# Performance work log

Hardware: AMD Instinct MI355X
Metric: run time of the kernel (lower is better)

## Reference

```python
import jax, jax.numpy as jnp
import numpy as np

N_HEADS, D_MODEL, D_HEAD = 16, 1024, 64
INIT_STD = 0.02


def setup_inputs() -> dict:
    key = jax.random.key(0)
    ks = jax.random.split(key, 5)
    x = jax.random.normal(ks[0], (4, 2048, D_MODEL), dtype=jnp.float32)
    W_Q = jax.random.normal(ks[1], (N_HEADS, D_MODEL, D_HEAD), dtype=jnp.float32) * INIT_STD
    W_K = jax.random.normal(ks[2], (N_HEADS, D_MODEL, D_HEAD), dtype=jnp.float32) * INIT_STD
    W_V = jax.random.normal(ks[3], (N_HEADS, D_MODEL, D_HEAD), dtype=jnp.float32) * INIT_STD
    W_O = jax.random.normal(ks[4], (N_HEADS, D_HEAD, D_MODEL), dtype=jnp.float32) * INIT_STD
    b_Q = jnp.zeros((N_HEADS, D_HEAD), dtype=jnp.float32)
    b_K = jnp.zeros((N_HEADS, D_HEAD), dtype=jnp.float32)
    b_V = jnp.zeros((N_HEADS, D_HEAD), dtype=jnp.float32)
    b_O = jnp.zeros((D_MODEL,), dtype=jnp.float32)
    return {"normalized_resid_pre": x, "W_Q": W_Q, "W_K": W_K, "W_V": W_V,
            "W_O": W_O, "b_Q": b_Q, "b_K": b_K, "b_V": b_V, "b_O": b_O}


def reference(normalized_resid_pre, W_Q, W_K, W_V, W_O, b_Q, b_K, b_V, b_O):
    x = normalized_resid_pre  # [b, s, d_model]
    q = jnp.einsum('bsm,hmd->bshd', x, W_Q) + b_Q  # [b, s, h, d_head]
    k = jnp.einsum('bsm,hmd->bshd', x, W_K) + b_K
    v = jnp.einsum('bsm,hmd->bshd', x, W_V) + b_V
    scores = jnp.einsum('bqhd,bkhd->bhqk', q, k) / jnp.sqrt(jnp.float32(D_HEAD))
    S = x.shape[1]
    causal = jnp.tril(jnp.ones((S, S), dtype=bool))  # keep key_pos <= query_pos
    scores = jnp.where(causal, scores, jnp.finfo(scores.dtype).min)
    pattern = jax.nn.softmax(scores, axis=-1)  # [b, h, q, k]
    z = jnp.einsum('bhqk,bkhd->bqhd', pattern, v)
    attn_out = jnp.einsum('bqhd,hdm->bqm', z, W_O) + b_O
    return attn_out
```

## Files before the change

### kernel.cpp

```cpp
#include <hip/hip_runtime.h>
#include <hip/hip_bf16.h>
#include <math.h>

typedef __bf16 bf16_t;
typedef bf16_t bf16x8 __attribute__((ext_vector_type(8)));
typedef float f32x4 __attribute__((ext_vector_type(4)));

#define BB 4
#define SS 2048
#define HH 16
#define DMODEL 1024
#define DHEAD 64

__device__ inline unsigned short f2bf(float f) {
    union { __hip_bfloat16 h; unsigned short u; } cvt;
    cvt.h = __float2bfloat16(f);
    return cvt.u;
}

__device__ __forceinline__ void gll16(const unsigned short* g, unsigned short* l) {
    __builtin_amdgcn_global_load_lds(
        (const __attribute__((address_space(1))) unsigned int*)(g),
        (__attribute__((address_space(3))) unsigned int*)(l), 16, 0, 0);
}


__global__ void pack_x(const float* __restrict__ x, unsigned short* __restrict__ xb) {
    int i = blockIdx.x * 256 + threadIdx.x;
    const float4 v = ((const float4*)x)[i];
    unsigned short o[4] = { f2bf(v.x), f2bf(v.y), f2bf(v.z), f2bf(v.w) };
    *(uint2*)(xb + 4 * (size_t)i) = *(uint2*)o;
}

__global__ void pack_wqkv(const float* __restrict__ wq, const float* __restrict__ wk,
                          const float* __restrict__ wv, unsigned short* __restrict__ out) {
    int idx = blockIdx.x * 256 + threadIdx.x;
    int k  = idx & 1023;
    int n  = idx >> 10;
    int mat = n >> 10;
    int n1 = n & 1023;
    int h = n1 >> 6, d = n1 & 63;
    const float* w = (mat == 0) ? wq : (mat == 1) ? wk : wv;
    out[idx] = f2bf(w[(h << 16) + (k << 6) + d]);
}

__global__ void pack_wo(const float* __restrict__ wo, unsigned short* __restrict__ out) {
    int idx = blockIdx.x * 256 + threadIdx.x;
    int k = idx & 1023, n = idx >> 10;
    out[idx] = f2bf(wo[(k << 10) + n]);
}


__global__ __launch_bounds__(256) void gemm_qkv(
    const unsigned short* __restrict__ xb,
    const unsigned short* __restrict__ wT,
    const float* __restrict__ bq, const float* __restrict__ bk, const float* __restrict__ bv,
    unsigned short* __restrict__ qws, unsigned short* __restrict__ kws,
    unsigned short* __restrict__ vtw)
{
    __shared__ __align__(16) unsigned short lA[128 * 32];
    __shared__ __align__(16) unsigned short lB[128 * 32];
    const int t = threadIdx.x;
    const int lane = t & 63;
    const int w = t >> 6;
    const int quad = lane >> 4;
    const int l15 = lane & 15;
    const int n0 = blockIdx.x * 128;
    const int m0 = blockIdx.y * 128;
    const int wm = (w >> 1) * 64;
    const int wn = (w & 1) * 64;
    const int mat = n0 >> 10;

    f32x4 acc[4][4] = {};

    const int srow = w * 16 + (lane >> 2);
    const int scol = (lane & 3) * 8;
    const unsigned short* Ag0 = xb + (size_t)(m0 + srow) * 1024 + scol;
    const unsigned short* Ag1 = Ag0 + (size_t)64 * 1024;
    const unsigned short* Bg0 = wT + (size_t)(n0 + srow) * 1024 + scol;
    const unsigned short* Bg1 = Bg0 + (size_t)64 * 1024;
    unsigned short* lA0 = lA + (w * 16) * 32;
    unsigned short* lA1 = lA + (64 + w * 16) * 32;
    unsigned short* lB0 = lB + (w * 16) * 32;
    unsigned short* lB1 = lB + (64 + w * 16) * 32;

    if (mat != 2) {
        for (int kt = 0; kt < 1024; kt += 32) {
            __syncthreads();
            gll16(Ag0 + kt, lA0);
            gll16(Ag1 + kt, lA1);
            gll16(Bg0 + kt, lB0);
            gll16(Bg1 + kt, lB1);
            __syncthreads();
            bf16x8 af[4], bfr[4];
#pragma unroll
            for (int i = 0; i < 4; i++) {
                af[i]  = *(const bf16x8*)(lA + (wm + i * 16 + l15) * 32 + quad * 8);
                bfr[i] = *(const bf16x8*)(lB + (wn + i * 16 + l15) * 32 + quad * 8);
            }
#pragma unroll
            for (int i = 0; i < 4; i++)
#pragma unroll
                for (int j = 0; j < 4; j++)
                    acc[i][j] = __builtin_amdgcn_mfma_f32_16x16x32_bf16(bfr[j], af[i], acc[i][j], 0, 0, 0);
        }
        const int b = m0 >> 11;
        const float* bias_p = (mat == 0) ? bq : bk;
        unsigned short* dst = (mat == 0) ? qws : kws;
#pragma unroll
        for (int j = 0; j < 4; j++) {
            const int noff = wn + j * 16 + quad * 4;
            const int h = noff >> 6;
            const int hglob = ((n0 & 1023) >> 6) + h;
            const int dbase = noff & 63;
            const float4 bv4 = *(const float4*)(bias_p + hglob * 64 + dbase);
            const float bias_r[4] = { bv4.x, bv4.y, bv4.z, bv4.w };
#pragma unroll
            for (int i = 0; i < 4; i++) {
                const int s = (m0 & 2047) + wm + i * 16 + l15;
                unsigned short pk[4];
#pragma unroll
                for (int r = 0; r < 4; r++) pk[r] = f2bf(acc[i][j][r] + bias_r[r]);
                *(uint2*)(dst + (size_t)((b * 16 + hglob) * 2048 + s) * 64 + dbase) = *(uint2*)pk;
            }
        }
    } else {
        for (int kt = 0; kt < 1024; kt += 32) {
            __syncthreads();
            gll16(Ag0 + kt, lA0);
            gll16(Ag1 + kt, lA1);
            gll16(Bg0 + kt, lB0);
            gll16(Bg1 + kt, lB1);
            __syncthreads();
            bf16x8 af[4], bfr[4];
#pragma unroll
            for (int i = 0; i < 4; i++) {
                af[i]  = *(const bf16x8*)(lA + (wm + i * 16 + l15) * 32 + quad * 8);
                bfr[i] = *(const bf16x8*)(lB + (wn + i * 16 + l15) * 32 + quad * 8);
            }
#pragma unroll
            for (int i = 0; i < 4; i++)
#pragma unroll
                for (int j = 0; j < 4; j++)
                    acc[i][j] = __builtin_amdgcn_mfma_f32_16x16x32_bf16(af[i], bfr[j], acc[i][j], 0, 0, 0);
        }
        const int b = m0 >> 11;
#pragma unroll
        for (int j = 0; j < 4; j++) {
            const int n1 = (n0 & 1023) + wn + j * 16 + l15;
            const int h = n1 >> 6, d = n1 & 63;
            const float bias = bv[h * 64 + d];
#pragma unroll
            for (int i = 0; i < 4; i++) {
                const int s0 = (m0 & 2047) + wm + i * 16 + quad * 4;
                unsigned short pk[4];
#pragma unroll
                for (int r = 0; r < 4; r++) pk[r] = f2bf(acc[i][j][r] + bias);
                *(uint2*)(vtw + ((size_t)(b * 16 + h) * 64 + d) * 2048 + s0) = *(uint2*)pk;
            }
        }
    }
}


__global__ __launch_bounds__(256) void attn3(
    const unsigned short* __restrict__ qws,
    const unsigned short* __restrict__ kws,
    const unsigned short* __restrict__ vtw,
    unsigned short* __restrict__ zb)
{
    __shared__ __align__(16) unsigned short Ks[64 * 72];
    __shared__ __align__(16) unsigned short Vs[64 * 72];
    __shared__ __align__(16) unsigned short Ps[4 * 16 * 72];

    const int t = threadIdx.x;
    const int lane = t & 63;
    const int w = t >> 6;
    const int quad = lane >> 4;
    const int l15 = lane & 15;

    const int qt = 31 - (blockIdx.x >> 6);
    const int bh = blockIdx.x & 63;
    const int q0 = qt * 64;
    const int qbase = q0 + w * 16;
    const size_t base = (size_t)bh * SS * DHEAD;
    const unsigned short* Q = qws + base;
    const unsigned short* K = kws + base;
    const unsigned short* Vt = vtw + base;

    bf16x8 qf0 = *(const bf16x8*)(Q + (size_t)(qbase + l15) * 64 + quad * 8);
    bf16x8 qf1 = *(const bf16x8*)(Q + (size_t)(qbase + l15) * 64 + 32 + quad * 8);

    f32x4 o[4] = {};
    float lsum[4] = {0.f, 0.f, 0.f, 0.f};
    unsigned short* Pw = Ps + w * 16 * 72;

    const int sr = t >> 2;
    const int sc = (t & 3) * 8;
    const int nch = qt + 1;

    for (int c = 0; c < nch; c++) {
        const int kb = c * 64;
        __syncthreads();
        {
            const unsigned short* kp = K + (size_t)(kb + sr) * 64 + sc;
            *(uint4*)(Ks + sr * 72 + sc)      = *(const uint4*)(kp);
            *(uint4*)(Ks + sr * 72 + sc + 32) = *(const uint4*)(kp + 32);
            const unsigned short* vp = Vt + (size_t)sr * 2048 + kb + sc;
            *(uint4*)(Vs + sr * 72 + sc)      = *(const uint4*)(vp);
            *(uint4*)(Vs + sr * 72 + sc + 32) = *(const uint4*)(vp + 32);
        }
        __syncthreads();

        f32x4 s[4];
#pragma unroll
        for (int sub = 0; sub < 4; sub++) {
            bf16x8 kf0 = *(const bf16x8*)(Ks + (sub * 16 + l15) * 72 + quad * 8);
            bf16x8 kf1 = *(const bf16x8*)(Ks + (sub * 16 + l15) * 72 + 32 + quad * 8);
            f32x4 sv = {};
            sv = __builtin_amdgcn_mfma_f32_16x16x32_bf16(qf0, kf0, sv, 0, 0, 0);
            sv = __builtin_amdgcn_mfma_f32_16x16x32_bf16(qf1, kf1, sv, 0, 0, 0);
            s[sub] = sv;
        }

        if (c == nch - 1) {
            const int qg = qbase + quad * 4;
#pragma unroll
            for (int sub = 0; sub < 4; sub++) {
                const int key = kb + sub * 16 + l15;
#pragma unroll
                for (int r = 0; r < 4; r++) {
                    float p = (key > qg + r) ? 0.f : __expf(s[sub][r] * 0.125f);
                    lsum[r] += p;
                    Pw[(quad * 4 + r) * 72 + sub * 16 + l15] = f2bf(p);
                }
            }
        } else {
#pragma unroll
            for (int sub = 0; sub < 4; sub++)
#pragma unroll
                for (int r = 0; r < 4; r++) {
                    float p = __expf(s[sub][r] * 0.125f);
                    lsum[r] += p;
                    Pw[(quad * 4 + r) * 72 + sub * 16 + l15] = f2bf(p);
                }
        }
        asm volatile("s_waitcnt lgkmcnt(0)" ::: "memory");
        bf16x8 pf0 = *(const bf16x8*)(Pw + l15 * 72 + quad * 8);
        bf16x8 pf1 = *(const bf16x8*)(Pw + l15 * 72 + 32 + quad * 8);
#pragma unroll
        for (int dt = 0; dt < 4; dt++) {
            bf16x8 vf0 = *(const bf16x8*)(Vs + (dt * 16 + l15) * 72 + quad * 8);
            bf16x8 vf1 = *(const bf16x8*)(Vs + (dt * 16 + l15) * 72 + 32 + quad * 8);
            o[dt] = __builtin_amdgcn_mfma_f32_16x16x32_bf16(vf0, pf0, o[dt], 0, 0, 0);
            o[dt] = __builtin_amdgcn_mfma_f32_16x16x32_bf16(vf1, pf1, o[dt], 0, 0, 0);
        }
    }

#pragma unroll
    for (int r = 0; r < 4; r++) {
        float v = lsum[r];
        v += __shfl_xor(v, 1);
        v += __shfl_xor(v, 2);
        v += __shfl_xor(v, 4);
        v += __shfl_xor(v, 8);
        lsum[r] = v;
    }
    const int srcl = (l15 >> 2) << 4;
    float t0 = __shfl(lsum[0], srcl);
    float t1 = __shfl(lsum[1], srcl);
    float t2 = __shfl(lsum[2], srcl);
    float t3 = __shfl(lsum[3], srcl);
    const int rr = l15 & 3;
    float den = (rr == 0) ? t0 : (rr == 1) ? t1 : (rr == 2) ? t2 : t3;
    const float inv = 1.0f / den;

    const int b = bh >> 4, h = bh & 15;
    const int q = qbase + l15;
    unsigned short* zrow = zb + (size_t)(b * 2048 + q) * 1024 + h * 64 + quad * 4;
#pragma unroll
    for (int dt = 0; dt < 4; dt++) {
        unsigned short pk[4];
#pragma unroll
        for (int r = 0; r < 4; r++) pk[r] = f2bf(o[dt][r] * inv);
        *(uint2*)(zrow + dt * 16) = *(uint2*)pk;
    }
}


__global__ __launch_bounds__(256) void gemm_out(
    const unsigned short* __restrict__ zb,
    const unsigned short* __restrict__ wT,
    const float* __restrict__ bo,
    float* __restrict__ out)
{
    __shared__ __align__(16) unsigned short lA[128 * 32];
    __shared__ __align__(16) unsigned short lB[128 * 32];
    const int t = threadIdx.x;
    const int lane = t & 63;
    const int w = t >> 6;
    const int quad = lane >> 4;
    const int l15 = lane & 15;
    const int n0 = blockIdx.x * 128;
    const int m0 = blockIdx.y * 128;
    const int wm = (w >> 1) * 64;
    const int wn = (w & 1) * 64;

    f32x4 acc[4][4] = {};

    const int srow = w * 16 + (lane >> 2);
    const int scol = (lane & 3) * 8;
    const unsigned short* Ag0 = zb + (size_t)(m0 + srow) * 1024 + scol;
    const unsigned short* Ag1 = Ag0 + (size_t)64 * 1024;
    const unsigned short* Bg0 = wT + (size_t)(n0 + srow) * 1024 + scol;
    const unsigned short* Bg1 = Bg0 + (size_t)64 * 1024;
    unsigned short* lA0 = lA + (w * 16) * 32;
    unsigned short* lA1 = lA + (64 + w * 16) * 32;
    unsigned short* lB0 = lB + (w * 16) * 32;
    unsigned short* lB1 = lB + (64 + w * 16) * 32;

    for (int kt = 0; kt < 1024; kt += 32) {
        __syncthreads();
        gll16(Ag0 + kt, lA0);
        gll16(Ag1 + kt, lA1);
        gll16(Bg0 + kt, lB0);
        gll16(Bg1 + kt, lB1);
        __syncthreads();
        bf16x8 af[4], bfr[4];
#pragma unroll
        for (int i = 0; i < 4; i++) {
            af[i]  = *(const bf16x8*)(lA + (wm + i * 16 + l15) * 32 + quad * 8);
            bfr[i] = *(const bf16x8*)(lB + (wn + i * 16 + l15) * 32 + quad * 8);
        }
#pragma unroll
        for (int i = 0; i < 4; i++)
#pragma unroll
            for (int j = 0; j < 4; j++)
                acc[i][j] = __builtin_amdgcn_mfma_f32_16x16x32_bf16(bfr[j], af[i], acc[i][j], 0, 0, 0);
    }

#pragma unroll
    for (int j = 0; j < 4; j++) {
        const int nbase = n0 + wn + j * 16 + quad * 4;
        const float4 bv4 = *(const float4*)(bo + nbase);
#pragma unroll
        for (int i = 0; i < 4; i++) {
            const int s = m0 + wm + i * 16 + l15;
            float4 v;
            v.x = acc[i][j][0] + bv4.x;
            v.y = acc[i][j][1] + bv4.y;
            v.z = acc[i][j][2] + bv4.z;
            v.w = acc[i][j][3] + bv4.w;
            *(float4*)(out + (size_t)s * 1024 + nbase) = v;
        }
    }
}


extern "C" void kernel_launch(void* const* d_in, const int* in_sizes, int n_in,
                              void* d_out, int out_size, void* d_ws, size_t ws_size,
                              hipStream_t stream) {
    const float* x  = (const float*)d_in[0];
    const float* WQ = (const float*)d_in[1];
    const float* WK = (const float*)d_in[2];
    const float* WV = (const float*)d_in[3];
    const float* WO = (const float*)d_in[4];
    const float* bQ = (const float*)d_in[5];
    const float* bK = (const float*)d_in[6];
    const float* bV = (const float*)d_in[7];
    const float* bO = (const float*)d_in[8];
    float* out = (float*)d_out;

    char* ws = (char*)d_ws;
    unsigned short* xb   = (unsigned short*)ws;
    unsigned short* wqkv = (unsigned short*)(ws + (16u << 20));
    unsigned short* woT  = (unsigned short*)(ws + (22u << 20));
    unsigned short* qws  = (unsigned short*)(ws + (24u << 20));
    unsigned short* kws  = (unsigned short*)(ws + (40u << 20));
    unsigned short* vtw  = (unsigned short*)(ws + (56u << 20));
    unsigned short* zbuf = xb;

    pack_x<<<8192, 256, 0, stream>>>(x, xb);
    pack_wqkv<<<(3072 * 1024) / 256, 256, 0, stream>>>(WQ, WK, WV, wqkv);
    pack_wo<<<(1024 * 1024) / 256, 256, 0, stream>>>(WO, woT);
    gemm_qkv<<<dim3(24, 64), 256, 0, stream>>>(xb, wqkv, bQ, bK, bV, qws, kws, vtw);
    attn3<<<2048, 256, 0, stream>>>(qws, kws, vtw, zbuf);
    gemm_out<<<dim3(8, 64), 256, 0, stream>>>(zbuf, woT, bO, out);
}
```

Measured before the change: 290.5 us.

## Double query rows per attention block and fold softmax scale into Q projection

The attention kernel now processes 128 query rows per block (32 per wave, as two 16-row tiles), so each K/V tile staged in shared memory is reused by twice as many queries, and the grid is halved. The score MFMA operand order is swapped so each lane holds the scores for one query row, which lets the row sum reduce with two cross-lane shuffles and lets probabilities be packed and written to LDS as whole vectors. The 1/sqrt(d_head) scale is applied once in the QKV GEMM epilogue instead of per score. The trade-offs are higher register pressure, waves idling on skipped causal chunks while still joining the block-wide syncs, and fewer blocks to balance the triangular workload.

```diff
diff --git a/kernel.cpp b/kernel.cpp
--- a/kernel.cpp
+++ b/kernel.cpp
@@ -107,6 +107,7 @@
         const int b = m0 >> 11;
         const float* bias_p = (mat == 0) ? bq : bk;
         unsigned short* dst = (mat == 0) ? qws : kws;
+        const float qscale = (mat == 0) ? 0.125f : 1.0f;
 #pragma unroll
         for (int j = 0; j < 4; j++) {
             const int noff = wn + j * 16 + quad * 4;
@@ -120,7 +121,7 @@
                 const int s = (m0 & 2047) + wm + i * 16 + l15;
                 unsigned short pk[4];
 #pragma unroll
-                for (int r = 0; r < 4; r++) pk[r] = f2bf(acc[i][j][r] + bias_r[r]);
+                for (int r = 0; r < 4; r++) pk[r] = f2bf((acc[i][j][r] + bias_r[r]) * qscale);
                 *(uint2*)(dst + (size_t)((b * 16 + hglob) * 2048 + s) * 64 + dbase) = *(uint2*)pk;
             }
         }
@@ -163,7 +164,7 @@
 }
 
 
-__global__ __launch_bounds__(256) void attn3(
+__global__ __launch_bounds__(256) void attn5(
     const unsigned short* __restrict__ qws,
     const unsigned short* __restrict__ kws,
     const unsigned short* __restrict__ vtw,
@@ -179,25 +180,30 @@
     const int quad = lane >> 4;
     const int l15 = lane & 15;
 
-    const int qt = 31 - (blockIdx.x >> 6);
+    const int qt = 15 - (blockIdx.x >> 6);
     const int bh = blockIdx.x & 63;
-    const int q0 = qt * 64;
-    const int qbase = q0 + w * 16;
+    const int q0 = qt * 128;
+    const int qbase = q0 + w * 32;
     const size_t base = (size_t)bh * SS * DHEAD;
     const unsigned short* Q = qws + base;
     const unsigned short* K = kws + base;
     const unsigned short* Vt = vtw + base;
 
-    bf16x8 qf0 = *(const bf16x8*)(Q + (size_t)(qbase + l15) * 64 + quad * 8);
-    bf16x8 qf1 = *(const bf16x8*)(Q + (size_t)(qbase + l15) * 64 + 32 + quad * 8);
-
-    f32x4 o[4] = {};
-    float lsum[4] = {0.f, 0.f, 0.f, 0.f};
+    bf16x8 qf[2][2];
+#pragma unroll
+    for (int qt_ = 0; qt_ < 2; qt_++) {
+        const unsigned short* qp = Q + (size_t)(qbase + qt_ * 16 + l15) * 64 + quad * 8;
+        qf[qt_][0] = *(const bf16x8*)(qp);
+        qf[qt_][1] = *(const bf16x8*)(qp + 32);
+    }
+
+    f32x4 o[2][4] = {};
+    float lsum[2] = {0.f, 0.f};
     unsigned short* Pw = Ps + w * 16 * 72;
 
     const int sr = t >> 2;
     const int sc = (t & 3) * 8;
-    const int nch = qt + 1;
+    const int nch = qt * 2 + 2;
 
     for (int c = 0; c < nch; c++) {
         const int kb = c * 64;
@@ -212,78 +218,84 @@
         }
         __syncthreads();
 
-        f32x4 s[4];
+        if (kb > qbase + 31) continue;
+
+        f32x4 st[2][4];
 #pragma unroll
         for (int sub = 0; sub < 4; sub++) {
-            bf16x8 kf0 = *(const bf16x8*)(Ks + (sub * 16 + l15) * 72 + quad * 8);
-            bf16x8 kf1 = *(const bf16x8*)(Ks + (sub * 16 + l15) * 72 + 32 + quad * 8);
-            f32x4 sv = {};
-            sv = __builtin_amdgcn_mfma_f32_16x16x32_bf16(qf0, kf0, sv, 0, 0, 0);
-            sv = __builtin_amdgcn_mfma_f32_16x16x32_bf16(qf1, kf1, sv, 0, 0, 0);
-            s[sub] = sv;
-        }
-
-        if (c == nch - 1) {
-            const int qg = qbase + quad * 4;
+            const bf16x8 kf0 = *(const bf16x8*)(Ks + (sub * 16 + l15) * 72 + quad * 8);
+            const bf16x8 kf1 = *(const bf16x8*)(Ks + (sub * 16 + l15) * 72 + 32 + quad * 8);
+#pragma unroll
+            for (int qt_ = 0; qt_ < 2; qt_++) {
+                f32x4 sv = {};
+                sv = __builtin_amdgcn_mfma_f32_16x16x32_bf16(kf0, qf[qt_][0], sv, 0, 0, 0);
+                sv = __builtin_amdgcn_mfma_f32_16x16x32_bf16(kf1, qf[qt_][1], sv, 0, 0, 0);
+                st[qt_][sub] = sv;
+            }
+        }
+
+        uint2 pd[2][4];
+        const bool edge = (kb + 63 > qbase);
+#pragma unroll
+        for (int qt_ = 0; qt_ < 2; qt_++) {
+            const int qg = qbase + qt_ * 16 + l15;
+            float psum = 0.f;
 #pragma unroll
             for (int sub = 0; sub < 4; sub++) {
-                const int key = kb + sub * 16 + l15;
+                float p[4];
 #pragma unroll
                 for (int r = 0; r < 4; r++) {
-                    float p = (key > qg + r) ? 0.f : __expf(s[sub][r] * 0.125f);
-                    lsum[r] += p;
-                    Pw[(quad * 4 + r) * 72 + sub * 16 + l15] = f2bf(p);
+                    const int key = kb + sub * 16 + quad * 4 + r;
+                    float v = __expf(st[qt_][sub][r]);
+                    p[r] = (edge && key > qg) ? 0.f : v;
+                    psum += p[r];
                 }
-            }
-        } else {
+                pd[qt_][sub].x = (unsigned)f2bf(p[0]) | ((unsigned)f2bf(p[1]) << 16);
+                pd[qt_][sub].y = (unsigned)f2bf(p[2]) | ((unsigned)f2bf(p[3]) << 16);
+            }
+            lsum[qt_] += psum;
+        }
+
+        bf16x8 vf[2][4];
+#pragma unroll
+        for (int c0 = 0; c0 < 2; c0++)
+#pragma unroll
+            for (int dt = 0; dt < 4; dt++)
+                vf[c0][dt] = *(const bf16x8*)(Vs + (dt * 16 + l15) * 72 + c0 * 32 + quad * 8);
+
+#pragma unroll
+        for (int qt_ = 0; qt_ < 2; qt_++) {
 #pragma unroll
             for (int sub = 0; sub < 4; sub++)
-#pragma unroll
-                for (int r = 0; r < 4; r++) {
-                    float p = __expf(s[sub][r] * 0.125f);
-                    lsum[r] += p;
-                    Pw[(quad * 4 + r) * 72 + sub * 16 + l15] = f2bf(p);
-                }
-        }
-        asm volatile("s_waitcnt lgkmcnt(0)" ::: "memory");
-        bf16x8 pf0 = *(const bf16x8*)(Pw + l15 * 72 + quad * 8);
-        bf16x8 pf1 = *(const bf16x8*)(Pw + l15 * 72 + 32 + quad * 8);
+                *(uint2*)(Pw + l15 * 72 + sub * 16 + quad * 4) = pd[qt_][sub];
+            asm volatile("s_waitcnt lgkmcnt(0)" ::: "memory");
+#pragma unroll
+            for (int c0 = 0; c0 < 2; c0++) {
+                const bf16x8 pf = *(const bf16x8*)(Pw + l15 * 72 + c0 * 32 + quad * 8);
+#pragma unroll
+                for (int dt = 0; dt < 4; dt++)
+                    o[qt_][dt] = __builtin_amdgcn_mfma_f32_16x16x32_bf16(vf[c0][dt], pf, o[qt_][dt], 0, 0, 0);
+            }
+            if (qt_ == 0) asm volatile("s_waitcnt lgkmcnt(0)" ::: "memory");
+        }
+    }
+
+    const int b = bh >> 4, h = bh & 15;
+#pragma unroll
+    for (int qt_ = 0; qt_ < 2; qt_++) {
+        float v = lsum[qt_];
+        v += __shfl_xor(v, 16);
+        v += __shfl_xor(v, 32);
+        const float inv = 1.0f / v;
+        const int q = qbase + qt_ * 16 + l15;
+        unsigned short* zrow = zb + (size_t)(b * 2048 + q) * 1024 + h * 64 + quad * 4;
 #pragma unroll
         for (int dt = 0; dt < 4; dt++) {
-            bf16x8 vf0 = *(const bf16x8*)(Vs + (dt * 16 + l15) * 72 + quad * 8);
-            bf16x8 vf1 = *(const bf16x8*)(Vs + (dt * 16 + l15) * 72 + 32 + quad * 8);
-            o[dt] = __builtin_amdgcn_mfma_f32_16x16x32_bf16(vf0, pf0, o[dt], 0, 0, 0);
-            o[dt] = __builtin_amdgcn_mfma_f32_16x16x32_bf16(vf1, pf1, o[dt], 0, 0, 0);
-        }
-    }
-
-#pragma unroll
-    for (int r = 0; r < 4; r++) {
-        float v = lsum[r];
-        v += __shfl_xor(v, 1);
-        v += __shfl_xor(v, 2);
-        v += __shfl_xor(v, 4);
-        v += __shfl_xor(v, 8);
-        lsum[r] = v;
-    }
-    const int srcl = (l15 >> 2) << 4;
-    float t0 = __shfl(lsum[0], srcl);
-    float t1 = __shfl(lsum[1], srcl);
-    float t2 = __shfl(lsum[2], srcl);
-    float t3 = __shfl(lsum[3], srcl);
-    const int rr = l15 & 3;
-    float den = (rr == 0) ? t0 : (rr == 1) ? t1 : (rr == 2) ? t2 : t3;
-    const float inv = 1.0f / den;
-
-    const int b = bh >> 4, h = bh & 15;
-    const int q = qbase + l15;
-    unsigned short* zrow = zb + (size_t)(b * 2048 + q) * 1024 + h * 64 + quad * 4;
-#pragma unroll
-    for (int dt = 0; dt < 4; dt++) {
-        unsigned short pk[4];
-#pragma unroll
-        for (int r = 0; r < 4; r++) pk[r] = f2bf(o[dt][r] * inv);
-        *(uint2*)(zrow + dt * 16) = *(uint2*)pk;
+            unsigned short pk[4];
+#pragma unroll
+            for (int r = 0; r < 4; r++) pk[r] = f2bf(o[qt_][dt][r] * inv);
+            *(uint2*)(zrow + dt * 16) = *(uint2*)pk;
+        }
     }
 }
 
@@ -384,6 +396,6 @@
     pack_wqkv<<<(3072 * 1024) / 256, 256, 0, stream>>>(WQ, WK, WV, wqkv);
     pack_wo<<<(1024 * 1024) / 256, 256, 0, stream>>>(WO, woT);
     gemm_qkv<<<dim3(24, 64), 256, 0, stream>>>(xb, wqkv, bQ, bK, bV, qws, kws, vtw);
-    attn3<<<2048, 256, 0, stream>>>(qws, kws, vtw, zbuf);
+    attn5<<<1024, 256, 0, stream>>>(qws, kws, vtw, zbuf);
     gemm_out<<<dim3(8, 64), 256, 0, stream>>>(zbuf, woT, bO, out);
 }
```

Measured after the change: 293.0 us. Within noise of the previous version (+0.9%).
